# Optimization experiments

Measured on AMD Instinct MI355X. Metric: run time of the kernel, lower is better.

Reference implementation:

```python
import jax, jax.numpy as jnp
import numpy as np

N_NODES = 100000


def gcn_conv(x, src, dst, W, b, n_nodes):
    """PyG GCNConv: add self-loops, symmetric degree normalization, X W, scatter-add."""
    # Linear transform first (small out dim -> cheaper messages)
    h = x @ W  # [N, F_out]
    # Add self-loops
    loop = jnp.arange(n_nodes, dtype=src.dtype)
    s = jnp.concatenate([src, loop])
    d = jnp.concatenate([dst, loop])
    # Degree (in-degree over dst, incl. self-loops), deg^{-1/2}
    deg = jax.ops.segment_sum(jnp.ones_like(d, dtype=h.dtype), d, num_segments=n_nodes)
    dinv = jnp.where(deg > 0, jax.lax.rsqrt(deg), 0.0)
    norm = dinv[s] * dinv[d]  # [E+N]
    # Gather-scale-scatter aggregation
    msgs = h[s] * norm[:, None]  # [E+N, F_out]
    out = jax.ops.segment_sum(msgs, d, num_segments=n_nodes)
    return out + b


def setup_inputs() -> dict:
    key = jax.random.key(0)
    ks = jax.random.split(key, 4)
    n, f_in, f_hid, f_out = N_NODES, 512, 16, 7
    n_edges = 3200000
    x = jax.random.normal(ks[0], (n, f_in), dtype=jnp.float32)
    edge_index = jax.random.randint(ks[1], (2, n_edges), 0, n, dtype=jnp.int64)
    W1 = jax.random.normal(ks[2], (f_in, f_hid), dtype=jnp.float32) / np.sqrt(f_in)
    b1 = jnp.zeros((f_hid,), dtype=jnp.float32)
    W2 = jax.random.normal(ks[3], (f_hid, f_out), dtype=jnp.float32) / np.sqrt(f_hid)
    b2 = jnp.zeros((f_out,), dtype=jnp.float32)
    return {"x": x, "edge_index": edge_index, "W1": W1, "b1": b1, "W2": W2, "b2": b2}


def reference(x, edge_index, W1, b1, W2, b2):
    n = x.shape[0]
    src, dst = edge_index[0], edge_index[1]
    h = gcn_conv(x, src, dst, W1, b1, n)
    h = jax.nn.relu(h)
    out = gcn_conv(h, src, dst, W2, b2, n)
    return out
```

## Files before the change

### kernel.cpp

```cpp
#include <hip/hip_runtime.h>

#define F_IN 512
#define F_HID 16
#define F_OUT 7
#define BUCKET 128
#define LB 7
#define TRASH 128
#define PADV 128
#define CHUNK 4096
#define MAXNB 1024

#define RPB 256
#define KC 32
#define KHALF 256
#define LSTRIDE 33

typedef int   int4v   __attribute__((ext_vector_type(4)));
typedef float float4v __attribute__((ext_vector_type(4)));
typedef unsigned int uint4v __attribute__((ext_vector_type(4)));

static __device__ __forceinline__ unsigned short f2bf(float f) {
    unsigned int u = __float_as_uint(f);
    u += 0x7FFFu + ((u >> 16) & 1u);
    return (unsigned short)(u >> 16);
}
static __device__ __forceinline__ float bf2f(unsigned short s) {
    return __uint_as_float((unsigned int)s << 16);
}

__global__ __launch_bounds__(256) void k_hist(const int* __restrict__ dst,
                                              int* __restrict__ bh, int E, int NB, int NBA) {
    __shared__ int hist[MAXNB];
    int t = threadIdx.x, blk = blockIdx.x;
    for (int i = t; i < NB; i += 256) hist[i] = 0;
    __syncthreads();
    int base = blk * CHUNK;
#pragma unroll
    for (int it = 0; it < CHUNK / 1024; ++it) {
        int e = base + (it * 256 + t) * 4;
        if (e < E) {
            int4v d4 = __builtin_nontemporal_load((const int4v*)(dst + e));
            atomicAdd(&hist[d4.x >> LB], 1);
            atomicAdd(&hist[d4.y >> LB], 1);
            atomicAdd(&hist[d4.z >> LB], 1);
            atomicAdd(&hist[d4.w >> LB], 1);
        }
    }
    __syncthreads();
    int* row = bh + (size_t)blk * NBA;
    for (int i = t; i < NB; i += 256) row[i] = hist[i];
}

__global__ __launch_bounds__(64) void k_cscan(int* __restrict__ bh, int* __restrict__ bucket_cnt,
                                              int PBLK, int NBA) {
    int i = blockIdx.x;
    int lane = threadIdx.x;
    int carry = 0;
    for (int k0 = 0; k0 < PBLK; k0 += 64) {
        int b = k0 + lane;
        int v = (b < PBLK) ? bh[(size_t)b * NBA + i] : 0;
        int s = v;
#pragma unroll
        for (int off = 1; off < 64; off <<= 1) {
            int u = __shfl_up(s, off);
            if (lane >= off) s += u;
        }
        if (b < PBLK) bh[(size_t)b * NBA + i] = carry + s - v;
        carry += __shfl(s, 63);
    }
    if (lane == 0) bucket_cnt[i] = carry;
}

__global__ void k_bscan1(const int* __restrict__ bucket_cnt, int* __restrict__ bucket_base,
                         int* __restrict__ bedges, int NB) {
    __shared__ int sm[MAXNB];
    int t = threadIdx.x;
    int c = (t < NB) ? bucket_cnt[t] : 0;
    int ca = (c + 3) & ~3;
    sm[t] = ca;
    __syncthreads();
    for (int off = 1; off < MAXNB; off <<= 1) {
        int v = sm[t];
        int add = (t >= off) ? sm[t - off] : 0;
        __syncthreads();
        sm[t] = v + add;
        __syncthreads();
    }
    if (t < NB) {
        int base = sm[t] - ca;
        bucket_base[t] = base;
        for (int i = c; i < ca; ++i) bedges[base + i] = PADV;
    }
}

__global__ __launch_bounds__(256) void k_place3(
        const int* __restrict__ src, const int* __restrict__ dst,
        const int* __restrict__ bucket_base, const int* __restrict__ bh,
        int* __restrict__ bedges, int E, int NB, int NBA) {
    __shared__ int h[MAXNB];
    __shared__ int s[MAXNB];
    __shared__ int sedge[CHUNK];
    __shared__ unsigned short sbkt[CHUNK];
    int t = threadIdx.x, blk = blockIdx.x;
    for (int i = t; i < MAXNB; i += 256) h[i] = 0;
    __syncthreads();
    int base = blk * CHUNK;
    int4v d4[4], s4[4];
#pragma unroll
    for (int it = 0; it < 4; ++it) {
        int e = base + (it * 256 + t) * 4;
        if (e < E) {
            d4[it] = __builtin_nontemporal_load((const int4v*)(dst + e));
            s4[it] = __builtin_nontemporal_load((const int4v*)(src + e));
        } else {
            int sent = NB << LB;
            d4[it].x = sent; d4[it].y = sent; d4[it].z = sent; d4[it].w = sent;
            s4[it].x = 0;    s4[it].y = 0;    s4[it].z = 0;    s4[it].w = 0;
        }
        atomicAdd(&h[d4[it].x >> LB], 1);
        atomicAdd(&h[d4[it].y >> LB], 1);
        atomicAdd(&h[d4[it].z >> LB], 1);
        atomicAdd(&h[d4[it].w >> LB], 1);
    }
    __syncthreads();
    for (int i = t; i < MAXNB; i += 256) s[i] = h[i];
    __syncthreads();
    for (int off = 1; off < MAXNB; off <<= 1) {
        int v[4];
#pragma unroll
        for (int j = 0; j < 4; ++j) {
            int i = t + j * 256;
            v[j] = s[i] + ((i >= off) ? s[i - off] : 0);
        }
        __syncthreads();
#pragma unroll
        for (int j = 0; j < 4; ++j) s[t + j * 256] = v[j];
        __syncthreads();
    }
    const int* row = bh + (size_t)blk * NBA;
    for (int i = t; i < MAXNB; i += 256) {
        int excl = s[i] - h[i];
        h[i] = excl;
        s[i] = (i < NB) ? (bucket_base[i] + row[i] - excl) : 0;
    }
    __syncthreads();
#pragma unroll
    for (int it = 0; it < 4; ++it) {
        int d, sv, b, p;
        d = d4[it].x; sv = s4[it].x; b = d >> LB; p = atomicAdd(&h[b], 1);
        sedge[p] = (sv << 8) | (d & (BUCKET - 1)); sbkt[p] = (unsigned short)b;
        d = d4[it].y; sv = s4[it].y; b = d >> LB; p = atomicAdd(&h[b], 1);
        sedge[p] = (sv << 8) | (d & (BUCKET - 1)); sbkt[p] = (unsigned short)b;
        d = d4[it].z; sv = s4[it].z; b = d >> LB; p = atomicAdd(&h[b], 1);
        sedge[p] = (sv << 8) | (d & (BUCKET - 1)); sbkt[p] = (unsigned short)b;
        d = d4[it].w; sv = s4[it].w; b = d >> LB; p = atomicAdd(&h[b], 1);
        sedge[p] = (sv << 8) | (d & (BUCKET - 1)); sbkt[p] = (unsigned short)b;
    }
    __syncthreads();
    for (int j = t; j < CHUNK; j += 256) {
        int b = sbkt[j];
        if (b < NB)
            __builtin_nontemporal_store(sedge[j], bedges + s[b] + j);
    }
}

__global__ void k_pcount(const int* __restrict__ bucket_base, const int* __restrict__ bucket_cnt,
                         const int* __restrict__ bedges, float* __restrict__ dinv,
                         int* __restrict__ node_off, int* __restrict__ bucket_psize, int n) {
    __shared__ int cnt[TRASH + 8];
    __shared__ int sc[BUCKET];
    int b = blockIdx.x, t = threadIdx.x;
    for (int i = t; i < TRASH + 8; i += 256) cnt[i] = 0;
    __syncthreads();
    int base = bucket_base[b], ne = bucket_cnt[b];
    int nqq = (ne + 3) >> 2;
    for (int qi = t; qi < nqq; qi += 256) {
        int4v q = __builtin_nontemporal_load((const int4v*)(bedges + base + (qi << 2)));
        atomicAdd(&cnt[q.x & 255], 1);
        atomicAdd(&cnt[q.y & 255], 1);
        atomicAdd(&cnt[q.z & 255], 1);
        atomicAdd(&cnt[q.w & 255], 1);
    }
    __syncthreads();
    int p = 0;
    if (t < BUCKET) { p = (cnt[t] + 3) & ~3; sc[t] = p; }
    __syncthreads();
    for (int off = 1; off < BUCKET; off <<= 1) {
        int v = 0;
        if (t < BUCKET) { v = sc[t]; if (t >= off) v += sc[t - off]; }
        __syncthreads();
        if (t < BUCKET) sc[t] = v;
        __syncthreads();
    }
    if (t < BUCKET) {
        int node = b * BUCKET + t;
        if (node < n) {
            dinv[node] = rsqrtf((float)(cnt[t] + 1));
            node_off[node] = sc[t] - p;
        }
        if (t == BUCKET - 1) bucket_psize[b] = sc[t];
    }
}

__global__ void k_bscan2(const int* __restrict__ bucket_psize, int* __restrict__ pbase, int NB) {
    __shared__ int sm[MAXNB];
    int t = threadIdx.x;
    int c = (t < NB) ? bucket_psize[t] : 0;
    sm[t] = c;
    __syncthreads();
    for (int off = 1; off < MAXNB; off <<= 1) {
        int v = sm[t];
        int add = (t >= off) ? sm[t - off] : 0;
        __syncthreads();
        sm[t] = v + add;
        __syncthreads();
    }
    if (t < NB) pbase[t] = sm[t] - c;
}

__global__ void k_sort(const int* __restrict__ bucket_base, const int* __restrict__ bucket_cnt,
                       const int* __restrict__ pbase, const int* __restrict__ bedges,
                       int* __restrict__ bedges2, int* __restrict__ node_off,
                       int* __restrict__ node_nq, int n) {
    __shared__ int cur[BUCKET];
    __shared__ int woffs[BUCKET];
    int b = blockIdx.x, t = threadIdx.x;
    int pb = pbase[b];
    if (t < BUCKET) {
        int node = b * BUCKET + t;
        int w = (node < n) ? node_off[node] : 0;
        woffs[t] = w;
        cur[t] = w;
    }
    __syncthreads();
    int base = bucket_base[b], ne = bucket_cnt[b];
    int nqq = (ne + 3) >> 2;
    for (int qi = t; qi < nqq; qi += 256) {
        int4v q = __builtin_nontemporal_load((const int4v*)(bedges + base + (qi << 2)));
        int v, dl, pos;
        v = q.x; dl = v & 255;
        if (dl < BUCKET) { pos = atomicAdd(&cur[dl], 1); bedges2[pb + pos] = v >> 8; }
        v = q.y; dl = v & 255;
        if (dl < BUCKET) { pos = atomicAdd(&cur[dl], 1); bedges2[pb + pos] = v >> 8; }
        v = q.z; dl = v & 255;
        if (dl < BUCKET) { pos = atomicAdd(&cur[dl], 1); bedges2[pb + pos] = v >> 8; }
        v = q.w; dl = v & 255;
        if (dl < BUCKET) { pos = atomicAdd(&cur[dl], 1); bedges2[pb + pos] = v >> 8; }
    }
    __syncthreads();
    if (t < BUCKET) {
        int node = b * BUCKET + t;
        if (node < n) {
            int w = woffs[t];
            int endc = cur[t];
            int cnt = endc - w;
            int p = (cnt + 3) & ~3;
            for (int i = endc; i < w + p; ++i) bedges2[pb + i] = n;
            node_off[node] = pb + w;
            node_nq[node] = p >> 2;
        }
    }
}

__global__ __launch_bounds__(256) void k_gemm1p(
        const float* __restrict__ x, const float* __restrict__ W,
        float* __restrict__ part, int n) {
    __shared__ float xs[RPB * LSTRIDE];
    int b  = blockIdx.x >> 1;
    int ks = blockIdx.x & 1;
    int r0 = b * RPB;
    int t  = threadIdx.x;
    int r  = r0 + t;
    int kbase = ks * KHALF;

    float acc[F_HID];
#pragma unroll
    for (int c = 0; c < F_HID; ++c) acc[c] = 0.0f;

    int lr0 = t >> 3;
    int c4  = t & 7;

    for (int kc = 0; kc < KHALF; kc += KC) {
        __syncthreads();
#pragma unroll
        for (int j = 0; j < 8; ++j) {
            int lr = j * 32 + lr0;
            int gr = r0 + lr;
            float4v v = {0.0f, 0.0f, 0.0f, 0.0f};
            if (gr < n)
                v = *(const float4v*)(x + (size_t)gr * F_IN + kbase + kc + c4 * 4);
            float* d = xs + lr * LSTRIDE + c4 * 4;
            d[0] = v.x; d[1] = v.y; d[2] = v.z; d[3] = v.w;
        }
        __syncthreads();
        if (r < n) {
            const float* xrow = xs + t * LSTRIDE;
            const float* Wk = W + (size_t)(kbase + kc) * F_HID;
#pragma unroll
            for (int k = 0; k < KC; ++k) {
                float xv = xrow[k];
#pragma unroll
                for (int c = 0; c < F_HID; ++c)
                    acc[c] = fmaf(xv, Wk[k * F_HID + c], acc[c]);
            }
        }
    }
    if (r < n) {
        float4v* o = (float4v*)(part + ((size_t)ks * n + r) * F_HID);
        float4v w0 = {acc[0],  acc[1],  acc[2],  acc[3]};
        float4v w1 = {acc[4],  acc[5],  acc[6],  acc[7]};
        float4v w2 = {acc[8],  acc[9],  acc[10], acc[11]};
        float4v w3 = {acc[12], acc[13], acc[14], acc[15]};
        o[0] = w0; o[1] = w1; o[2] = w2; o[3] = w3;
    }
}

__global__ void k_fin1(const float* __restrict__ part, const float* __restrict__ dinv,
                       unsigned short* __restrict__ h1b, int n) {
    int tg = blockIdx.x * 256 + threadIdx.x;
    int r = tg >> 4, c = tg & 15;
    if (r > n) return;
    if (r == n) { h1b[(size_t)r * F_HID + c] = 0; return; }
    float v = part[(size_t)r * F_HID + c] + part[((size_t)n + r) * F_HID + c];
    h1b[(size_t)r * F_HID + c] = f2bf(dinv[r] * v);
}

__global__ __launch_bounds__(1024) void k_agg1(
        const int* __restrict__ node_off, const int* __restrict__ node_nq,
        const int* __restrict__ bedges2, const unsigned short* __restrict__ h1b,
        const float* __restrict__ dinv, float* __restrict__ agg1, int n) {
    int tg = blockIdx.x * 1024 + threadIdx.x;
    int node = tg >> 4, c = tg & 15;
    if (node >= n) return;
    int off = node_off[node], nq = node_nq[node];
    float acc = bf2f(h1b[(size_t)node * F_HID + c]);
    for (int q = 0; q < nq; ++q) {
        int4v s = *(const int4v*)(bedges2 + off + (q << 2));
        float v0 = bf2f(h1b[(size_t)s.x * F_HID + c]);
        float v1 = bf2f(h1b[(size_t)s.y * F_HID + c]);
        float v2 = bf2f(h1b[(size_t)s.z * F_HID + c]);
        float v3 = bf2f(h1b[(size_t)s.w * F_HID + c]);
        acc += v0 + v1 + v2 + v3;
    }
    agg1[(size_t)node * F_HID + c] = dinv[node] * acc;
}

__global__ void k_layer2(const float* __restrict__ agg1, const float* __restrict__ b1,
                         const float* __restrict__ W2, const float* __restrict__ dinv,
                         unsigned short* __restrict__ h2b, int n) {
    int r = blockIdx.x * blockDim.x + threadIdx.x;
    if (r > n) return;
    if (r == n) {
        uint4v z = {0u, 0u, 0u, 0u};
        *(uint4v*)(h2b + (size_t)r * 8) = z;
        return;
    }
    float z[F_HID];
    const float4* ai = (const float4*)(agg1 + (size_t)r * F_HID);
#pragma unroll
    for (int q = 0; q < 4; ++q) {
        float4 v = ai[q];
        z[q * 4 + 0] = fmaxf(v.x + b1[q * 4 + 0], 0.0f);
        z[q * 4 + 1] = fmaxf(v.y + b1[q * 4 + 1], 0.0f);
        z[q * 4 + 2] = fmaxf(v.z + b1[q * 4 + 2], 0.0f);
        z[q * 4 + 3] = fmaxf(v.w + b1[q * 4 + 3], 0.0f);
    }
    float h[F_OUT];
#pragma unroll
    for (int c = 0; c < F_OUT; ++c) h[c] = 0.0f;
#pragma unroll
    for (int k = 0; k < F_HID; ++k)
#pragma unroll
        for (int c = 0; c < F_OUT; ++c)
            h[c] = fmaf(z[k], W2[k * F_OUT + c], h[c]);
    float dv = dinv[r];
    uint4v w;
    w.x = (unsigned)f2bf(dv * h[0]) | ((unsigned)f2bf(dv * h[1]) << 16);
    w.y = (unsigned)f2bf(dv * h[2]) | ((unsigned)f2bf(dv * h[3]) << 16);
    w.z = (unsigned)f2bf(dv * h[4]) | ((unsigned)f2bf(dv * h[5]) << 16);
    w.w = (unsigned)f2bf(dv * h[6]);
    *(uint4v*)(h2b + (size_t)r * 8) = w;
}

__global__ __launch_bounds__(1024) void k_agg2(
        const int* __restrict__ node_off, const int* __restrict__ node_nq,
        const int* __restrict__ bedges2, const unsigned short* __restrict__ h2b,
        const float* __restrict__ dinv, const float* __restrict__ b2,
        float* __restrict__ out, int n) {
    int tg = blockIdx.x * 1024 + threadIdx.x;
    int node = tg >> 3, c = tg & 7;
    if (node >= n) return;
    int off = node_off[node], nq = node_nq[node];
    float acc = bf2f(h2b[(size_t)node * 8 + c]);
    for (int q = 0; q < nq; ++q) {
        int4v s = *(const int4v*)(bedges2 + off + (q << 2));
        float v0 = bf2f(h2b[(size_t)s.x * 8 + c]);
        float v1 = bf2f(h2b[(size_t)s.y * 8 + c]);
        float v2 = bf2f(h2b[(size_t)s.z * 8 + c]);
        float v3 = bf2f(h2b[(size_t)s.w * 8 + c]);
        acc += v0 + v1 + v2 + v3;
    }
    if (c < F_OUT)
        out[(size_t)node * F_OUT + c] = dinv[node] * acc + b2[c];
}

extern "C" void kernel_launch(void* const* d_in, const int* in_sizes, int n_in,
                              void* d_out, int out_size, void* d_ws, size_t ws_size,
                              hipStream_t stream) {
    const float* x  = (const float*)d_in[0];
    const int*   ei = (const int*)d_in[1];
    const float* W1 = (const float*)d_in[2];
    const float* b1 = (const float*)d_in[3];
    const float* W2 = (const float*)d_in[4];
    const float* b2 = (const float*)d_in[5];
    float* out = (float*)d_out;

    const int n = in_sizes[0] / F_IN;
    const int E = in_sizes[1] / 2;
    const int* src = ei;
    const int* dst = ei + E;

    const int NB = (n + BUCKET - 1) / BUCKET;
    const int NBA = (NB + 3) & ~3;
    const int PBLK = (E + CHUNK - 1) / CHUNK;

    size_t Np = ((size_t)n + 3) & ~(size_t)3;
    char* ws = (char*)d_ws;
    int*   bucket_cnt   = (int*)ws;             ws += MAXNB * 4;
    int*   bucket_base  = (int*)ws;             ws += MAXNB * 4;
    int*   bucket_psize = (int*)ws;             ws += MAXNB * 4;
    int*   pbase        = (int*)ws;             ws += MAXNB * 4;
    int*   bh           = (int*)ws;             ws += (size_t)PBLK * NBA * 4;
    float* dinv         = (float*)ws;           ws += Np * 4;
    int*   node_off     = (int*)ws;             ws += Np * 4;
    int*   node_nq      = (int*)ws;             ws += Np * 4;
    int*   bedges       = (int*)ws;             ws += ((size_t)E + 4 * MAXNB) * 4;
    int*   bedges2      = (int*)ws;             ws += ((size_t)E + 4 * Np) * 4;
    unsigned short* h1b = (unsigned short*)ws;  ws += (Np + 4) * F_HID * 2;
    float* part         = (float*)bedges;
    float* agg1         = (float*)bedges;
    unsigned short* h2b = h1b;

    k_hist   <<<PBLK, 256, 0, stream>>>(dst, bh, E, NB, NBA);
    k_cscan  <<<NB, 64, 0, stream>>>(bh, bucket_cnt, PBLK, NBA);
    k_bscan1 <<<1, 1024, 0, stream>>>(bucket_cnt, bucket_base, bedges, NB);
    k_place3 <<<PBLK, 256, 0, stream>>>(src, dst, bucket_base, bh, bedges, E, NB, NBA);
    k_pcount <<<NB, 256, 0, stream>>>(bucket_base, bucket_cnt, bedges, dinv, node_off, bucket_psize, n);
    k_bscan2 <<<1, 1024, 0, stream>>>(bucket_psize, pbase, NB);
    k_sort   <<<NB, 256, 0, stream>>>(bucket_base, bucket_cnt, pbase, bedges, bedges2, node_off, node_nq, n);
    k_gemm1p <<<((n + RPB - 1) / RPB) * 2, 256, 0, stream>>>(x, W1, part, n);
    k_fin1   <<<((n + 1) * 16 + 255) / 256, 256, 0, stream>>>(part, dinv, h1b, n);
    k_agg1   <<<((size_t)n * 16 + 1023) / 1024, 1024, 0, stream>>>(node_off, node_nq, bedges2, h1b, dinv, agg1, n);
    k_layer2 <<<(n + 1 + 255) / 256, 256, 0, stream>>>(agg1, b1, W2, dinv, h2b, n);
    k_agg2   <<<((size_t)n * 8 + 1023) / 1024, 1024, 0, stream>>>(node_off, node_nq, bedges2, h2b, dinv, b2, out, n);
}
```

Measured before the change: 470.0 us.

## Replace per-node CSR sort with bucket-level shared-memory atomic aggregation

Drops the second-level counting sort (k_bscan2, k_sort, node offsets) and aggregates directly from the bucketed edge list. Each block accumulates messages for its 128 destination nodes in shared memory with float atomics, and the layer-1 kernel folds bias, ReLU and the W2 projection in using a shuffle reduction. This removes a full pass that rewrites the edge array plus two kernels. The cost is LDS atomic contention, a fixed 128-node grid with one block per bucket that may load-balance worse, and a nondeterministic summation order. The GEMM inner loop is also changed to float2 vector FMAs.

Result: slower. 915.9 us (+94.9%).

```diff
diff --git a/kernel.cpp b/kernel.cpp
--- a/kernel.cpp
+++ b/kernel.cpp
@@ -16,6 +16,7 @@
 #define LSTRIDE 33
 
 typedef int   int4v   __attribute__((ext_vector_type(4)));
+typedef float float2v __attribute__((ext_vector_type(2)));
 typedef float float4v __attribute__((ext_vector_type(4)));
 typedef unsigned int uint4v __attribute__((ext_vector_type(4)));
 
@@ -164,11 +165,9 @@
     }
 }
 
-__global__ void k_pcount(const int* __restrict__ bucket_base, const int* __restrict__ bucket_cnt,
-                         const int* __restrict__ bedges, float* __restrict__ dinv,
-                         int* __restrict__ node_off, int* __restrict__ bucket_psize, int n) {
+__global__ void k_pcount2(const int* __restrict__ bucket_base, const int* __restrict__ bucket_cnt,
+                          const int* __restrict__ bedges, float* __restrict__ dinv, int n) {
     __shared__ int cnt[TRASH + 8];
-    __shared__ int sc[BUCKET];
     int b = blockIdx.x, t = threadIdx.x;
     for (int i = t; i < TRASH + 8; i += 256) cnt[i] = 0;
     __syncthreads();
@@ -182,83 +181,9 @@
         atomicAdd(&cnt[q.w & 255], 1);
     }
     __syncthreads();
-    int p = 0;
-    if (t < BUCKET) { p = (cnt[t] + 3) & ~3; sc[t] = p; }
-    __syncthreads();
-    for (int off = 1; off < BUCKET; off <<= 1) {
-        int v = 0;
-        if (t < BUCKET) { v = sc[t]; if (t >= off) v += sc[t - off]; }
-        __syncthreads();
-        if (t < BUCKET) sc[t] = v;
-        __syncthreads();
-    }
     if (t < BUCKET) {
         int node = b * BUCKET + t;
-        if (node < n) {
-            dinv[node] = rsqrtf((float)(cnt[t] + 1));
-            node_off[node] = sc[t] - p;
-        }
-        if (t == BUCKET - 1) bucket_psize[b] = sc[t];
-    }
-}
-
-__global__ void k_bscan2(const int* __restrict__ bucket_psize, int* __restrict__ pbase, int NB) {
-    __shared__ int sm[MAXNB];
-    int t = threadIdx.x;
-    int c = (t < NB) ? bucket_psize[t] : 0;
-    sm[t] = c;
-    __syncthreads();
-    for (int off = 1; off < MAXNB; off <<= 1) {
-        int v = sm[t];
-        int add = (t >= off) ? sm[t - off] : 0;
-        __syncthreads();
-        sm[t] = v + add;
-        __syncthreads();
-    }
-    if (t < NB) pbase[t] = sm[t] - c;
-}
-
-__global__ void k_sort(const int* __restrict__ bucket_base, const int* __restrict__ bucket_cnt,
-                       const int* __restrict__ pbase, const int* __restrict__ bedges,
-                       int* __restrict__ bedges2, int* __restrict__ node_off,
-                       int* __restrict__ node_nq, int n) {
-    __shared__ int cur[BUCKET];
-    __shared__ int woffs[BUCKET];
-    int b = blockIdx.x, t = threadIdx.x;
-    int pb = pbase[b];
-    if (t < BUCKET) {
-        int node = b * BUCKET + t;
-        int w = (node < n) ? node_off[node] : 0;
-        woffs[t] = w;
-        cur[t] = w;
-    }
-    __syncthreads();
-    int base = bucket_base[b], ne = bucket_cnt[b];
-    int nqq = (ne + 3) >> 2;
-    for (int qi = t; qi < nqq; qi += 256) {
-        int4v q = __builtin_nontemporal_load((const int4v*)(bedges + base + (qi << 2)));
-        int v, dl, pos;
-        v = q.x; dl = v & 255;
-        if (dl < BUCKET) { pos = atomicAdd(&cur[dl], 1); bedges2[pb + pos] = v >> 8; }
-        v = q.y; dl = v & 255;
-        if (dl < BUCKET) { pos = atomicAdd(&cur[dl], 1); bedges2[pb + pos] = v >> 8; }
-        v = q.z; dl = v & 255;
-        if (dl < BUCKET) { pos = atomicAdd(&cur[dl], 1); bedges2[pb + pos] = v >> 8; }
-        v = q.w; dl = v & 255;
-        if (dl < BUCKET) { pos = atomicAdd(&cur[dl], 1); bedges2[pb + pos] = v >> 8; }
-    }
-    __syncthreads();
-    if (t < BUCKET) {
-        int node = b * BUCKET + t;
-        if (node < n) {
-            int w = woffs[t];
-            int endc = cur[t];
-            int cnt = endc - w;
-            int p = (cnt + 3) & ~3;
-            for (int i = endc; i < w + p; ++i) bedges2[pb + i] = n;
-            node_off[node] = pb + w;
-            node_nq[node] = p >> 2;
-        }
+        if (node < n) dinv[node] = rsqrtf((float)(cnt[t] + 1));
     }
 }
 
@@ -273,9 +198,9 @@
     int r  = r0 + t;
     int kbase = ks * KHALF;
 
-    float acc[F_HID];
-#pragma unroll
-    for (int c = 0; c < F_HID; ++c) acc[c] = 0.0f;
+    float2v acc2[F_HID / 2];
+#pragma unroll
+    for (int c = 0; c < F_HID / 2; ++c) acc2[c] = (float2v){0.0f, 0.0f};
 
     int lr0 = t >> 3;
     int c4  = t & 7;
@@ -295,22 +220,23 @@
         __syncthreads();
         if (r < n) {
             const float* xrow = xs + t * LSTRIDE;
-            const float* Wk = W + (size_t)(kbase + kc) * F_HID;
+            const float2v* Wk2 = (const float2v*)(W + (size_t)(kbase + kc) * F_HID);
 #pragma unroll
             for (int k = 0; k < KC; ++k) {
                 float xv = xrow[k];
 #pragma unroll
-                for (int c = 0; c < F_HID; ++c)
-                    acc[c] = fmaf(xv, Wk[k * F_HID + c], acc[c]);
+                for (int c2 = 0; c2 < F_HID / 2; ++c2)
+                    acc2[c2] += xv * Wk2[k * (F_HID / 2) + c2];
             }
         }
     }
     if (r < n) {
+        const float* a = (const float*)acc2;
         float4v* o = (float4v*)(part + ((size_t)ks * n + r) * F_HID);
-        float4v w0 = {acc[0],  acc[1],  acc[2],  acc[3]};
-        float4v w1 = {acc[4],  acc[5],  acc[6],  acc[7]};
-        float4v w2 = {acc[8],  acc[9],  acc[10], acc[11]};
-        float4v w3 = {acc[12], acc[13], acc[14], acc[15]};
+        float4v w0 = {a[0],  a[1],  a[2],  a[3]};
+        float4v w1 = {a[4],  a[5],  a[6],  a[7]};
+        float4v w2 = {a[8],  a[9],  a[10], a[11]};
+        float4v w3 = {a[12], a[13], a[14], a[15]};
         o[0] = w0; o[1] = w1; o[2] = w2; o[3] = w3;
     }
 }
@@ -325,83 +251,76 @@
     h1b[(size_t)r * F_HID + c] = f2bf(dinv[r] * v);
 }
 
-__global__ __launch_bounds__(1024) void k_agg1(
-        const int* __restrict__ node_off, const int* __restrict__ node_nq,
-        const int* __restrict__ bedges2, const unsigned short* __restrict__ h1b,
-        const float* __restrict__ dinv, float* __restrict__ agg1, int n) {
-    int tg = blockIdx.x * 1024 + threadIdx.x;
-    int node = tg >> 4, c = tg & 15;
-    if (node >= n) return;
-    int off = node_off[node], nq = node_nq[node];
-    float acc = bf2f(h1b[(size_t)node * F_HID + c]);
-    for (int q = 0; q < nq; ++q) {
-        int4v s = *(const int4v*)(bedges2 + off + (q << 2));
-        float v0 = bf2f(h1b[(size_t)s.x * F_HID + c]);
-        float v1 = bf2f(h1b[(size_t)s.y * F_HID + c]);
-        float v2 = bf2f(h1b[(size_t)s.z * F_HID + c]);
-        float v3 = bf2f(h1b[(size_t)s.w * F_HID + c]);
-        acc += v0 + v1 + v2 + v3;
-    }
-    agg1[(size_t)node * F_HID + c] = dinv[node] * acc;
-}
-
-__global__ void k_layer2(const float* __restrict__ agg1, const float* __restrict__ b1,
-                         const float* __restrict__ W2, const float* __restrict__ dinv,
-                         unsigned short* __restrict__ h2b, int n) {
-    int r = blockIdx.x * blockDim.x + threadIdx.x;
-    if (r > n) return;
-    if (r == n) {
-        uint4v z = {0u, 0u, 0u, 0u};
-        *(uint4v*)(h2b + (size_t)r * 8) = z;
-        return;
-    }
-    float z[F_HID];
-    const float4* ai = (const float4*)(agg1 + (size_t)r * F_HID);
-#pragma unroll
-    for (int q = 0; q < 4; ++q) {
-        float4 v = ai[q];
-        z[q * 4 + 0] = fmaxf(v.x + b1[q * 4 + 0], 0.0f);
-        z[q * 4 + 1] = fmaxf(v.y + b1[q * 4 + 1], 0.0f);
-        z[q * 4 + 2] = fmaxf(v.z + b1[q * 4 + 2], 0.0f);
-        z[q * 4 + 3] = fmaxf(v.w + b1[q * 4 + 3], 0.0f);
-    }
-    float h[F_OUT];
-#pragma unroll
-    for (int c = 0; c < F_OUT; ++c) h[c] = 0.0f;
-#pragma unroll
-    for (int k = 0; k < F_HID; ++k)
-#pragma unroll
-        for (int c = 0; c < F_OUT; ++c)
-            h[c] = fmaf(z[k], W2[k * F_OUT + c], h[c]);
-    float dv = dinv[r];
-    uint4v w;
-    w.x = (unsigned)f2bf(dv * h[0]) | ((unsigned)f2bf(dv * h[1]) << 16);
-    w.y = (unsigned)f2bf(dv * h[2]) | ((unsigned)f2bf(dv * h[3]) << 16);
-    w.z = (unsigned)f2bf(dv * h[4]) | ((unsigned)f2bf(dv * h[5]) << 16);
-    w.w = (unsigned)f2bf(dv * h[6]);
-    *(uint4v*)(h2b + (size_t)r * 8) = w;
-}
-
-__global__ __launch_bounds__(1024) void k_agg2(
-        const int* __restrict__ node_off, const int* __restrict__ node_nq,
-        const int* __restrict__ bedges2, const unsigned short* __restrict__ h2b,
+__global__ __launch_bounds__(256) void k_aggL1(
+        const int* __restrict__ bucket_base, const int* __restrict__ bucket_cnt,
+        const int* __restrict__ bedges, const unsigned short* __restrict__ h1b,
+        const float* __restrict__ dinv, const float* __restrict__ b1,
+        const float* __restrict__ W2, unsigned short* __restrict__ h2b, int n) {
+    __shared__ float acc[BUCKET * F_HID];
+    int b = blockIdx.x, t = threadIdx.x;
+    for (int i = t; i < BUCKET * F_HID; i += 256) acc[i] = 0.0f;
+    __syncthreads();
+    int base = bucket_base[b];
+    int ne4 = (bucket_cnt[b] + 3) & ~3;
+    int g = t >> 4, c = t & 15;
+    for (int e = g; e < ne4; e += 16) {
+        int v = bedges[base + e];
+        int dl = v & 255;
+        if (dl < BUCKET) {
+            float x = bf2f(h1b[((size_t)(unsigned)(v >> 8) << 4) + c]);
+            unsafeAtomicAdd(&acc[dl * F_HID + c], x);
+        }
+    }
+    __syncthreads();
+    for (int nd = g; nd < BUCKET; nd += 16) {
+        int node = b * BUCKET + nd;
+        if (node < n) {
+            float dv = dinv[node];
+            float a = acc[nd * F_HID + c] + bf2f(h1b[((size_t)node << 4) + c]);
+            float z = fmaxf(dv * a + b1[c], 0.0f);
+            float h[F_OUT];
+#pragma unroll
+            for (int o = 0; o < F_OUT; ++o) h[o] = z * W2[c * F_OUT + o];
+#pragma unroll
+            for (int sft = 8; sft >= 1; sft >>= 1)
+#pragma unroll
+                for (int o = 0; o < F_OUT; ++o) h[o] += __shfl_xor(h[o], sft, 16);
+            if (c < 8) {
+                unsigned short w = (c < F_OUT) ? f2bf(dv * h[c]) : (unsigned short)0;
+                h2b[((size_t)node << 3) + c] = w;
+            }
+        }
+    }
+}
+
+__global__ __launch_bounds__(256) void k_aggL2(
+        const int* __restrict__ bucket_base, const int* __restrict__ bucket_cnt,
+        const int* __restrict__ bedges, const unsigned short* __restrict__ h2b,
         const float* __restrict__ dinv, const float* __restrict__ b2,
         float* __restrict__ out, int n) {
-    int tg = blockIdx.x * 1024 + threadIdx.x;
-    int node = tg >> 3, c = tg & 7;
-    if (node >= n) return;
-    int off = node_off[node], nq = node_nq[node];
-    float acc = bf2f(h2b[(size_t)node * 8 + c]);
-    for (int q = 0; q < nq; ++q) {
-        int4v s = *(const int4v*)(bedges2 + off + (q << 2));
-        float v0 = bf2f(h2b[(size_t)s.x * 8 + c]);
-        float v1 = bf2f(h2b[(size_t)s.y * 8 + c]);
-        float v2 = bf2f(h2b[(size_t)s.z * 8 + c]);
-        float v3 = bf2f(h2b[(size_t)s.w * 8 + c]);
-        acc += v0 + v1 + v2 + v3;
-    }
-    if (c < F_OUT)
-        out[(size_t)node * F_OUT + c] = dinv[node] * acc + b2[c];
+    __shared__ float acc[BUCKET * 8];
+    int b = blockIdx.x, t = threadIdx.x;
+    for (int i = t; i < BUCKET * 8; i += 256) acc[i] = 0.0f;
+    __syncthreads();
+    int base = bucket_base[b];
+    int ne4 = (bucket_cnt[b] + 3) & ~3;
+    int g = t >> 3, c = t & 7;
+    for (int e = g; e < ne4; e += 32) {
+        int v = bedges[base + e];
+        int dl = v & 255;
+        if (dl < BUCKET) {
+            float x = bf2f(h2b[((size_t)(unsigned)(v >> 8) << 3) + c]);
+            unsafeAtomicAdd(&acc[dl * 8 + c], x);
+        }
+    }
+    __syncthreads();
+    for (int nd = g; nd < BUCKET; nd += 32) {
+        int node = b * BUCKET + nd;
+        if (node < n && c < F_OUT) {
+            float a = acc[nd * 8 + c] + bf2f(h2b[((size_t)node << 3) + c]);
+            out[(size_t)node * F_OUT + c] = dinv[node] * a + b2[c];
+        }
+    }
 }
 
 extern "C" void kernel_launch(void* const* d_in, const int* in_sizes, int n_in,
@@ -428,29 +347,20 @@
     char* ws = (char*)d_ws;
     int*   bucket_cnt   = (int*)ws;             ws += MAXNB * 4;
     int*   bucket_base  = (int*)ws;             ws += MAXNB * 4;
-    int*   bucket_psize = (int*)ws;             ws += MAXNB * 4;
-    int*   pbase        = (int*)ws;             ws += MAXNB * 4;
     int*   bh           = (int*)ws;             ws += (size_t)PBLK * NBA * 4;
     float* dinv         = (float*)ws;           ws += Np * 4;
-    int*   node_off     = (int*)ws;             ws += Np * 4;
-    int*   node_nq      = (int*)ws;             ws += Np * 4;
     int*   bedges       = (int*)ws;             ws += ((size_t)E + 4 * MAXNB) * 4;
-    int*   bedges2      = (int*)ws;             ws += ((size_t)E + 4 * Np) * 4;
+    float* part         = (float*)ws;           ws += (size_t)2 * Np * F_HID * 4;
     unsigned short* h1b = (unsigned short*)ws;  ws += (Np + 4) * F_HID * 2;
-    float* part         = (float*)bedges;
-    float* agg1         = (float*)bedges;
-    unsigned short* h2b = h1b;
+    unsigned short* h2b = (unsigned short*)ws;  ws += (Np + 4) * 8 * 2;
 
     k_hist   <<<PBLK, 256, 0, stream>>>(dst, bh, E, NB, NBA);
     k_cscan  <<<NB, 64, 0, stream>>>(bh, bucket_cnt, PBLK, NBA);
     k_bscan1 <<<1, 1024, 0, stream>>>(bucket_cnt, bucket_base, bedges, NB);
     k_place3 <<<PBLK, 256, 0, stream>>>(src, dst, bucket_base, bh, bedges, E, NB, NBA);
-    k_pcount <<<NB, 256, 0, stream>>>(bucket_base, bucket_cnt, bedges, dinv, node_off, bucket_psize, n);
-    k_bscan2 <<<1, 1024, 0, stream>>>(bucket_psize, pbase, NB);
-    k_sort   <<<NB, 256, 0, stream>>>(bucket_base, bucket_cnt, pbase, bedges, bedges2, node_off, node_nq, n);
+    k_pcount2<<<NB, 256, 0, stream>>>(bucket_base, bucket_cnt, bedges, dinv, n);
     k_gemm1p <<<((n + RPB - 1) / RPB) * 2, 256, 0, stream>>>(x, W1, part, n);
     k_fin1   <<<((n + 1) * 16 + 255) / 256, 256, 0, stream>>>(part, dinv, h1b, n);
-    k_agg1   <<<((size_t)n * 16 + 1023) / 1024, 1024, 0, stream>>>(node_off, node_nq, bedges2, h1b, dinv, agg1, n);
-    k_layer2 <<<(n + 1 + 255) / 256, 256, 0, stream>>>(agg1, b1, W2, dinv, h2b, n);
-    k_agg2   <<<((size_t)n * 8 + 1023) / 1024, 1024, 0, stream>>>(node_off, node_nq, bedges2, h2b, dinv, b2, out, n);
-}
+    k_aggL1  <<<NB, 256, 0, stream>>>(bucket_base, bucket_cnt, bedges, h1b, dinv, b1, W2, h2b, n);
+    k_aggL2  <<<NB, 256, 0, stream>>>(bucket_base, bucket_cnt, bedges, h2b, dinv, b2, out, n);
+}
```
